# Kernel optimization log

Measured on AMD Instinct MI355X. Metric: run time of the kernel, lower is better.

## Reference

```python
import jax, jax.numpy as jnp
import numpy as np

N = 1_000_000          # atoms
D_IN = 118             # one-hot atom-type dim
D_OUT = 64             # embedded feature dim
NUM_SEG = 4096         # graphs in batch


def setup_inputs() -> dict:
    key = jax.random.key(0)
    k1, k2, k3, k4 = jax.random.split(key, 4)
    x = jax.random.normal(k1, (N, D_IN), dtype=jnp.float32)
    W = jax.random.normal(k2, (D_OUT, D_IN), dtype=jnp.float32) * (1.0 / np.sqrt(D_IN))
    b = jax.random.normal(k3, (D_OUT,), dtype=jnp.float32) * 0.01
    batch = jnp.sort(jax.random.randint(k4, (N,), 0, NUM_SEG, dtype=jnp.int64))
    return {"x": x, "W": W, "b": b, "batch": batch, "num_segments": NUM_SEG}


def reference(x, W, b, batch, num_segments):
    # linear + relu (per-atom embedding)
    h = jax.nn.relu(jnp.einsum("nd,od->no", x, W) + b)  # [N, D_OUT]
    # opaque inner model treated as identity
    # scatter_add over graph ids (segment reduce)
    s = jax.ops.segment_sum(h, batch, num_segments=num_segments)  # [G, D_OUT]
    s = jax.nn.relu(s)
    # max-normalize each graph's feature vector
    maxima = jnp.max(s, axis=1, keepdims=True)  # [G, 1]
    return s / maxima
```

## Files before the change

kernel.cpp:

```cpp
#include <hip/hip_runtime.h>
#include <hip/hip_bf16.h>
#include <stdint.h>

#define D_IN 118
#define D_OUT 64
#define KPAD 128
#define BM 128
#define XS_STRIDE 136

typedef __attribute__((ext_vector_type(8))) short bf16x8;
typedef __attribute__((ext_vector_type(4))) float floatx4;

__device__ __forceinline__ uint16_t f2bf(float f) {
    uint32_t u;
    __builtin_memcpy(&u, &f, 4);
    uint32_t r = (u + 0x7fffu + ((u >> 16) & 1u)) >> 16;
    return (uint16_t)r;
}

__device__ __forceinline__ uint32_t pack_bf16(float a, float b) {
    return (uint32_t)f2bf(a) | ((uint32_t)f2bf(b) << 16);
}

__global__ void wconv(const float* __restrict__ W, ushort* __restrict__ Wt) {
    int idx = blockIdx.x * 256 + threadIdx.x;
    if (idx >= D_OUT * KPAD) return;
    int o = idx >> 7, k = idx & 127;
    float v = (k < D_IN) ? W[o * D_IN + k] : 0.f;
    Wt[idx] = f2bf(v);
}

__global__ __launch_bounds__(256) void fused_main(
    const float* __restrict__ x, const ushort* __restrict__ Wt,
    const float* __restrict__ bias, const int* __restrict__ batch,
    float* __restrict__ out, int n_atoms)
{
    __shared__ __align__(16) ushort xs[BM * XS_STRIDE];
    __shared__ int ids[BM];

    const int tid = threadIdx.x;
    const int atom0 = blockIdx.x * BM;

    if (tid < BM) {
        int a = atom0 + tid;
        ids[tid] = (a < n_atoms) ? batch[a] : -1;
    }

#pragma unroll
    for (int ph = 0; ph < 8; ++ph) {
        int tau = ph * 256 + tid;
        int m = tau >> 4, c = tau & 15;
        long row = atom0 + m;
        bool rok = row < n_atoms;
        const float* src = x + row * D_IN + c * 8;
        uint32_t pk[4];
#pragma unroll
        for (int j = 0; j < 4; ++j) {
            int k = c * 8 + j * 2;
            float2 v = make_float2(0.f, 0.f);
            if (rok && k < D_IN) v = *reinterpret_cast<const float2*>(src + j * 2);
            pk[j] = pack_bf16(v.x, v.y);
        }
        *reinterpret_cast<uint4*>(&xs[m * XS_STRIDE + c * 8]) =
            make_uint4(pk[0], pk[1], pk[2], pk[3]);
    }

    const int lane = tid & 63;
    const int wv = tid >> 6;
    const int n = lane & 15;
    const int q = lane >> 4;

    bf16x8 bfrag[4][4];
#pragma unroll
    for (int ot = 0; ot < 4; ++ot)
#pragma unroll
        for (int ks = 0; ks < 4; ++ks) {
            const ushort* p = Wt + (ot * 16 + n) * KPAD + ks * 32 + q * 8;
            bfrag[ot][ks] = *reinterpret_cast<const bf16x8*>(p);
        }

    __syncthreads();

    floatx4 acc[2][4];
#pragma unroll
    for (int mt = 0; mt < 2; ++mt)
#pragma unroll
        for (int ot = 0; ot < 4; ++ot)
            acc[mt][ot] = (floatx4){0.f, 0.f, 0.f, 0.f};

#pragma unroll
    for (int ks = 0; ks < 4; ++ks) {
        bf16x8 afrag[2];
#pragma unroll
        for (int mt = 0; mt < 2; ++mt) {
            int row = wv * 32 + mt * 16 + n;
            afrag[mt] = *reinterpret_cast<const bf16x8*>(
                &xs[row * XS_STRIDE + ks * 32 + q * 8]);
        }
#pragma unroll
        for (int mt = 0; mt < 2; ++mt)
#pragma unroll
            for (int ot = 0; ot < 4; ++ot)
                acc[mt][ot] = __builtin_amdgcn_mfma_f32_16x16x32_bf16(
                    afrag[mt], bfrag[ot][ks], acc[mt][ot], 0, 0, 0);
    }

    float bv[4];
#pragma unroll
    for (int ot = 0; ot < 4; ++ot) bv[ot] = bias[ot * 16 + n];

    float racc[4] = {0.f, 0.f, 0.f, 0.f};
    int cur = ids[wv * 32 + q * 4];
#pragma unroll
    for (int mt = 0; mt < 2; ++mt) {
#pragma unroll
        for (int reg = 0; reg < 4; ++reg) {
            int r = wv * 32 + mt * 16 + q * 4 + reg;
            int id = ids[r];
            if (id != cur) {
                if (cur >= 0) {
#pragma unroll
                    for (int ot = 0; ot < 4; ++ot)
                        atomicAdd(&out[cur * 64 + ot * 16 + n], racc[ot]);
                }
                cur = id;
                racc[0] = racc[1] = racc[2] = racc[3] = 0.f;
            }
#pragma unroll
            for (int ot = 0; ot < 4; ++ot) {
                float h = acc[mt][ot][reg] + bv[ot];
                racc[ot] += fmaxf(h, 0.f);
            }
        }
    }
    if (cur >= 0) {
#pragma unroll
        for (int ot = 0; ot < 4; ++ot)
            atomicAdd(&out[cur * 64 + ot * 16 + n], racc[ot]);
    }
}

__global__ void finalize(float* __restrict__ out, int nseg) {
    int row = blockIdx.x * 4 + (threadIdx.x >> 6);
    int lane = threadIdx.x & 63;
    if (row >= nseg) return;
    float v = fmaxf(out[row * 64 + lane], 0.f);
    float m = v;
#pragma unroll
    for (int off = 32; off > 0; off >>= 1)
        m = fmaxf(m, __shfl_xor(m, off, 64));
    out[row * 64 + lane] = v / m;
}

extern "C" void kernel_launch(void* const* d_in, const int* in_sizes, int n_in,
                              void* d_out, int out_size, void* d_ws, size_t ws_size,
                              hipStream_t stream) {
    const float* x = (const float*)d_in[0];
    const float* W = (const float*)d_in[1];
    const float* b = (const float*)d_in[2];
    const int* batch = (const int*)d_in[3];
    int n_atoms = in_sizes[0] / D_IN;
    int nseg = out_size / D_OUT;
    float* out = (float*)d_out;
    ushort* Wt = (ushort*)d_ws;

    hipMemsetAsync(d_out, 0, (size_t)out_size * sizeof(float), stream);
    wconv<<<dim3((D_OUT * KPAD + 255) / 256), dim3(256), 0, stream>>>(W, Wt);
    int nblocks = (n_atoms + BM - 1) / BM;
    fused_main<<<dim3(nblocks), dim3(256), 0, stream>>>(x, Wt, b, batch, out, n_atoms);
    finalize<<<dim3((nseg + 3) / 4), dim3(256), 0, stream>>>(out, nseg);
}
```

Baseline: 696.7 us.

## Aggregate segments in LDS, vectorize x loads, fuse output zeroing into wconv

Each block now accumulates per-segment partial sums in a shared-memory buffer indexed relative to the block's first segment, then flushes non-zero entries to global memory with atomics. This cuts global atomic traffic. The x tile is loaded with float4 reads and packed to bf16 through a cheaper perm-based conversion that rounds half up instead of to even. W fragments are read from global memory inside the MFMA loop instead of being preloaded into registers, launch bounds now request 4 blocks per CU, and the memset is folded into the wconv kernel. The extra LDS, the added syncs and the changed bf16 rounding are the trade-offs.

```diff
diff --git a/kernel.cpp b/kernel.cpp
--- a/kernel.cpp
+++ b/kernel.cpp
@@ -7,6 +7,7 @@
 #define KPAD 128
 #define BM 128
 #define XS_STRIDE 136
+#define MAXSEG 16
 
 typedef __attribute__((ext_vector_type(8))) short bf16x8;
 typedef __attribute__((ext_vector_type(4))) float floatx4;
@@ -14,29 +15,38 @@
 __device__ __forceinline__ uint16_t f2bf(float f) {
     uint32_t u;
     __builtin_memcpy(&u, &f, 4);
-    uint32_t r = (u + 0x7fffu + ((u >> 16) & 1u)) >> 16;
-    return (uint16_t)r;
-}
-
-__device__ __forceinline__ uint32_t pack_bf16(float a, float b) {
-    return (uint32_t)f2bf(a) | ((uint32_t)f2bf(b) << 16);
-}
-
-__global__ void wconv(const float* __restrict__ W, ushort* __restrict__ Wt) {
+    return (uint16_t)((u + 0x7fffu + ((u >> 16) & 1u)) >> 16);
+}
+
+__device__ __forceinline__ uint32_t pack2(float a, float b) {
+    uint32_t ua, ub;
+    __builtin_memcpy(&ua, &a, 4);
+    __builtin_memcpy(&ub, &b, 4);
+    ua += 0x8000u;
+    ub += 0x8000u;
+    return __builtin_amdgcn_perm(ub, ua, 0x07060302);
+}
+
+__global__ void wconv(const float* __restrict__ W, ushort* __restrict__ Wt,
+                      float* __restrict__ out, int out_elems) {
     int idx = blockIdx.x * 256 + threadIdx.x;
-    if (idx >= D_OUT * KPAD) return;
-    int o = idx >> 7, k = idx & 127;
-    float v = (k < D_IN) ? W[o * D_IN + k] : 0.f;
-    Wt[idx] = f2bf(v);
-}
-
-__global__ __launch_bounds__(256) void fused_main(
+    if (idx < D_OUT * KPAD) {
+        int o = idx >> 7, k = idx & 127;
+        float v = (k < D_IN) ? W[o * D_IN + k] : 0.f;
+        Wt[idx] = f2bf(v);
+    }
+    for (int i = idx; i < out_elems; i += D_OUT * KPAD)
+        out[i] = 0.f;
+}
+
+__global__ __launch_bounds__(256, 4) void fused_main(
     const float* __restrict__ x, const ushort* __restrict__ Wt,
     const float* __restrict__ bias, const int* __restrict__ batch,
     float* __restrict__ out, int n_atoms)
 {
     __shared__ __align__(16) ushort xs[BM * XS_STRIDE];
     __shared__ int ids[BM];
+    __shared__ float segacc[MAXSEG * 64];
 
     const int tid = threadIdx.x;
     const int atom0 = blockIdx.x * BM;
@@ -45,6 +55,9 @@
         int a = atom0 + tid;
         ids[tid] = (a < n_atoms) ? batch[a] : -1;
     }
+#pragma unroll
+    for (int i = 0; i < (MAXSEG * 64) / 256; ++i)
+        segacc[i * 256 + tid] = 0.0f;
 
 #pragma unroll
     for (int ph = 0; ph < 8; ++ph) {
@@ -52,17 +65,32 @@
         int m = tau >> 4, c = tau & 15;
         long row = atom0 + m;
         bool rok = row < n_atoms;
-        const float* src = x + row * D_IN + c * 8;
-        uint32_t pk[4];
-#pragma unroll
-        for (int j = 0; j < 4; ++j) {
-            int k = c * 8 + j * 2;
-            float2 v = make_float2(0.f, 0.f);
-            if (rok && k < D_IN) v = *reinterpret_cast<const float2*>(src + j * 2);
-            pk[j] = pack_bf16(v.x, v.y);
-        }
-        *reinterpret_cast<uint4*>(&xs[m * XS_STRIDE + c * 8]) =
-            make_uint4(pk[0], pk[1], pk[2], pk[3]);
+        const float* src = x + row * (long)D_IN + c * 8;
+        float4 v0 = make_float4(0.f, 0.f, 0.f, 0.f);
+        float4 v1 = make_float4(0.f, 0.f, 0.f, 0.f);
+        if (rok) {
+            if (c < 14) {
+                v0 = *reinterpret_cast<const float4*>(src);
+                v1 = *reinterpret_cast<const float4*>(src + 4);
+            } else if (c == 14) {
+                v0 = *reinterpret_cast<const float4*>(src);
+                if (row + 1 < n_atoms) {
+                    v1 = *reinterpret_cast<const float4*>(src + 4);
+                    v1.z = 0.f;
+                    v1.w = 0.f;
+                } else {
+                    float2 t = *reinterpret_cast<const float2*>(src + 4);
+                    v1.x = t.x;
+                    v1.y = t.y;
+                }
+            }
+        }
+        uint4 pkd;
+        pkd.x = pack2(v0.x, v0.y);
+        pkd.y = pack2(v0.z, v0.w);
+        pkd.z = pack2(v1.x, v1.y);
+        pkd.w = pack2(v1.z, v1.w);
+        *reinterpret_cast<uint4*>(&xs[m * XS_STRIDE + c * 8]) = pkd;
     }
 
     const int lane = tid & 63;
@@ -70,15 +98,6 @@
     const int n = lane & 15;
     const int q = lane >> 4;
 
-    bf16x8 bfrag[4][4];
-#pragma unroll
-    for (int ot = 0; ot < 4; ++ot)
-#pragma unroll
-        for (int ks = 0; ks < 4; ++ks) {
-            const ushort* p = Wt + (ot * 16 + n) * KPAD + ks * 32 + q * 8;
-            bfrag[ot][ks] = *reinterpret_cast<const bf16x8*>(p);
-        }
-
     __syncthreads();
 
     floatx4 acc[2][4];
@@ -98,17 +117,21 @@
                 &xs[row * XS_STRIDE + ks * 32 + q * 8]);
         }
 #pragma unroll
-        for (int mt = 0; mt < 2; ++mt)
-#pragma unroll
-            for (int ot = 0; ot < 4; ++ot)
-                acc[mt][ot] = __builtin_amdgcn_mfma_f32_16x16x32_bf16(
-                    afrag[mt], bfrag[ot][ks], acc[mt][ot], 0, 0, 0);
+        for (int ot = 0; ot < 4; ++ot) {
+            bf16x8 bfrag = *reinterpret_cast<const bf16x8*>(
+                Wt + (ot * 16 + n) * KPAD + ks * 32 + q * 8);
+            acc[0][ot] = __builtin_amdgcn_mfma_f32_16x16x32_bf16(
+                afrag[0], bfrag, acc[0][ot], 0, 0, 0);
+            acc[1][ot] = __builtin_amdgcn_mfma_f32_16x16x32_bf16(
+                afrag[1], bfrag, acc[1][ot], 0, 0, 0);
+        }
     }
 
     float bv[4];
 #pragma unroll
     for (int ot = 0; ot < 4; ++ot) bv[ot] = bias[ot * 16 + n];
 
+    const int s_first = ids[0];
     float racc[4] = {0.f, 0.f, 0.f, 0.f};
     int cur = ids[wv * 32 + q * 4];
 #pragma unroll
@@ -119,24 +142,45 @@
             int id = ids[r];
             if (id != cur) {
                 if (cur >= 0) {
-#pragma unroll
-                    for (int ot = 0; ot < 4; ++ot)
-                        atomicAdd(&out[cur * 64 + ot * 16 + n], racc[ot]);
+                    int si = cur - s_first;
+                    if (si < MAXSEG) {
+#pragma unroll
+                        for (int ot = 0; ot < 4; ++ot)
+                            atomicAdd(&segacc[si * 64 + ot * 16 + n], racc[ot]);
+                    } else {
+#pragma unroll
+                        for (int ot = 0; ot < 4; ++ot)
+                            atomicAdd(&out[cur * 64 + ot * 16 + n], racc[ot]);
+                    }
                 }
                 cur = id;
                 racc[0] = racc[1] = racc[2] = racc[3] = 0.f;
             }
 #pragma unroll
-            for (int ot = 0; ot < 4; ++ot) {
-                float h = acc[mt][ot][reg] + bv[ot];
-                racc[ot] += fmaxf(h, 0.f);
-            }
+            for (int ot = 0; ot < 4; ++ot)
+                racc[ot] += fmaxf(acc[mt][ot][reg] + bv[ot], 0.f);
         }
     }
     if (cur >= 0) {
-#pragma unroll
-        for (int ot = 0; ot < 4; ++ot)
-            atomicAdd(&out[cur * 64 + ot * 16 + n], racc[ot]);
+        int si = cur - s_first;
+        if (si < MAXSEG) {
+#pragma unroll
+            for (int ot = 0; ot < 4; ++ot)
+                atomicAdd(&segacc[si * 64 + ot * 16 + n], racc[ot]);
+        } else {
+#pragma unroll
+            for (int ot = 0; ot < 4; ++ot)
+                atomicAdd(&out[cur * 64 + ot * 16 + n], racc[ot]);
+        }
+    }
+
+    __syncthreads();
+#pragma unroll
+    for (int i0 = 0; i0 < (MAXSEG * 64) / 256; ++i0) {
+        int i = i0 * 256 + tid;
+        float v = segacc[i];
+        if (v != 0.0f)
+            atomicAdd(&out[(s_first + (i >> 6)) * 64 + (i & 63)], v);
     }
 }
 
@@ -164,8 +208,7 @@
     float* out = (float*)d_out;
     ushort* Wt = (ushort*)d_ws;
 
-    hipMemsetAsync(d_out, 0, (size_t)out_size * sizeof(float), stream);
-    wconv<<<dim3((D_OUT * KPAD + 255) / 256), dim3(256), 0, stream>>>(W, Wt);
+    wconv<<<dim3(32), dim3(256), 0, stream>>>(W, Wt, out, out_size);
     int nblocks = (n_atoms + BM - 1) / BM;
     fused_main<<<dim3(nblocks), dim3(256), 0, stream>>>(x, Wt, b, batch, out, n_atoms);
     finalize<<<dim3((nseg + 3) / 4), dim3(256), 0, stream>>>(out, nseg);
```

Result: faster. 656.2 us (-5.8%).
